# Kernel optimization log

Hardware: AMD Instinct MI355X
Metric: run time of the kernel (lower is better)

The kernel has to match this reference:

```python
import jax, jax.numpy as jnp
import numpy as np

GRID = 256

def _build_edges(g):
    ii, jj = np.meshgrid(np.arange(g), np.arange(g), indexing='ij')
    center = ii * g + jj
    srcs, tgts, attrs = [], [], []
    for di in (-1, 0, 1):
        for dj in (-1, 0, 1):
            if di == 0 and dj == 0:
                continue
            ni, nj = ii + di, jj + dj
            m = (ni >= 0) & (ni < g) & (nj >= 0) & (nj < g)
            srcs.append(center[m])
            tgts.append((ni * g + nj)[m])
            n = int(m.sum())
            a = np.empty((n, 3), np.float32)
            a[:, 0] = np.sqrt(di * di + dj * dj)
            a[:, 1] = di
            a[:, 2] = dj
            attrs.append(a)
    return (np.concatenate(srcs).astype(np.int32),
            np.concatenate(tgts).astype(np.int32),
            np.concatenate(attrs, axis=0))

def setup_inputs() -> dict:
    key = jax.random.key(0)
    ks = jax.random.split(key, 16)
    B, T, C, g = 2, 5, 10, GRID
    width, kw, out_c, Hh = 64, 32, 10, 32
    src, tgt, attr = _build_edges(g)
    nrm = lambda k, s: 0.1 * jax.random.normal(k, s, dtype=jnp.float32)
    return {
        'x': nrm(ks[0], (B, T, C, g, g)),
        'edge_src': jnp.asarray(src),
        'edge_tgt': jnp.asarray(tgt),
        'edge_attr': jnp.asarray(attr),
        'Wih0': nrm(ks[1], (4 * Hh, C)),
        'Whh0': nrm(ks[2], (4 * Hh, Hh)),
        'bih0': nrm(ks[3], (4 * Hh,)),
        'bhh0': nrm(ks[4], (4 * Hh,)),
        'Wih1': nrm(ks[5], (4 * Hh, Hh)),
        'Whh1': nrm(ks[6], (4 * Hh, Hh)),
        'bih1': nrm(ks[7], (4 * Hh,)),
        'bhh1': nrm(ks[8], (4 * Hh,)),
        'fc1_w': nrm(ks[9], (width, Hh)),
        'fc1_b': nrm(ks[10], (width,)),
        'conv_w': nrm(ks[11], (4, width, width)),
        'conv_b': nrm(ks[12], (4, width)),
        'gparam': jnp.ones((4,), jnp.float32),
        'fc2_w': nrm(ks[13], (kw, width)),
        'fc2_b': nrm(ks[14], (kw,)),
        'fc3_w': nrm(ks[15], (out_c, kw)),
        'fc3_b': jnp.zeros((out_c,), jnp.float32),
    }

def _lstm_cell(xt, h, c, Wih, Whh, bih, bhh):
    z = xt @ Wih.T + bih + h @ Whh.T + bhh
    i, f, g, o = jnp.split(z, 4, axis=-1)  # torch gate order i,f,g,o
    c = jax.nn.sigmoid(f) * c + jax.nn.sigmoid(i) * jnp.tanh(g)
    h = jax.nn.sigmoid(o) * jnp.tanh(c)
    return h, c

def _forward(x, edge_src, edge_tgt, edge_attr, Wih0, Whh0, bih0, bhh0,
             Wih1, Whh1, bih1, bhh1, fc1_w, fc1_b, conv_w, conv_b, gparam,
             fc2_w, fc2_b, fc3_w, fc3_b):
    B, T, C, H, W = x.shape
    N = H * W
    Hh = Whh0.shape[1]
    # (B,T,C,H,W) -> (T, B*N, C) sequence for the temporal LSTM over every node
    seq = x.transpose(0, 3, 4, 1, 2).reshape(B * N, T, C).transpose(1, 0, 2)

    def step(carry, xt):
        h0, c0, h1, c1 = carry
        h0, c0 = _lstm_cell(xt, h0, c0, Wih0, Whh0, bih0, bhh0)
        h1, c1 = _lstm_cell(h0, h1, c1, Wih1, Whh1, bih1, bhh1)
        return (h0, c0, h1, c1), None

    z = jnp.zeros((B * N, Hh), x.dtype)
    (h0, c0, h1, c1), _ = jax.lax.scan(step, (z, z, z, z), seq)
    feats = jax.nn.relu(h1 @ fc1_w.T + fc1_b).reshape(B, N, -1)  # (B,N,width)

    dist2 = edge_attr[:, 0:1] ** 2  # (E,1)
    depth = conv_w.shape[0]
    for k in range(depth):
        gw = jnp.exp(-dist2 / (gparam[k] ** 2 + 1e-8))       # (E,1) gaussian gate
        msg = (feats[:, edge_src] @ conv_w[k]) * gw          # (B,E,width)
        agg = jnp.zeros_like(feats).at[:, edge_tgt].add(msg) # scatter-add per batch
        feats = agg + feats @ conv_w[k] + conv_b[k]
        if k != depth - 1:
            feats = jax.nn.relu(feats)

    out = jax.nn.relu(feats @ fc2_w.T + fc2_b) @ fc3_w.T + fc3_b  # (B,N,out_c)
    out = out.reshape(B, H, W, -1).transpose(0, 3, 1, 2)[:, None]  # (B,1,out_c,H,W)
    return out

def reference(x, edge_src, edge_tgt, edge_attr, Wih0, Whh0, bih0, bhh0,
              Wih1, Whh1, bih1, bhh1, fc1_w, fc1_b, conv_w, conv_b, gparam,
              fc2_w, fc2_b, fc3_w, fc3_b):
    return _forward(x, edge_src, edge_tgt, edge_attr, Wih0, Whh0, bih0, bhh0,
                    Wih1, Whh1, bih1, bhh1, fc1_w, fc1_b, conv_w, conv_b, gparam,
                    fc2_w, fc2_b, fc3_w, fc3_b)
```

## Files before the change

### kernel.cpp

```cpp
#include <hip/hip_runtime.h>
#include <hip/hip_bf16.h>

#define NPIX   65536
#define TT     5
#define CC     10
#define HH     32
#define WIDTH  64
#define KW     32
#define OUTC   10

#define OFF_L0I    0
#define OFF_L0H    1280
#define OFF_L1I    5376
#define OFF_L1H    9472
#define OFF_B0     13568
#define OFF_B1     13696
#define OFF_FC1W   13824
#define OFF_FC1B   15872
#define OFF_CWT2   16384
#define OFF_CB     32768
#define OFF_FC2W2  33024
#define OFF_FC2B   35072
#define OFF_FC3W4  35104
#define OFF_FC3B   35424
#define OFF_GW     35440
#define OFF_FEATS_A 36864
#define OFF_FEATS_B (36864 + 8388608)

#define STRAIGHT_ATTR_IDX (65025 * 3)

__device__ __forceinline__ float sigf(float x)  { return 1.0f / (1.0f + __expf(-x)); }
__device__ __forceinline__ float tanhf_(float x){ return 1.0f - 2.0f / (__expf(2.0f * x) + 1.0f); }

__global__ __launch_bounds__(256, 1)
void prep_kernel(const float* Wih0, const float* Whh0,
                 const float* bih0, const float* bhh0,
                 const float* Wih1, const float* Whh1,
                 const float* bih1, const float* bhh1,
                 const float* fc1w, const float* fc1b,
                 const float* convw, const float* convb,
                 const float* fc2w, const float* fc2b,
                 const float* fc3w, const float* fc3b,
                 const float* gparam, const float* eattr,
                 float* P) {
    int tid = blockIdx.x * blockDim.x + threadIdx.x;
    int stride = gridDim.x * blockDim.x;
    for (int idx = tid; idx < 1280; idx += stride) {
        int g = idx & 3, j = (idx >> 2) & 31, c = idx >> 7;
        P[OFF_L0I + idx] = Wih0[(g * 32 + j) * 10 + c];
    }
    for (int idx = tid; idx < 4096; idx += stride) {
        int g = idx & 3, j = (idx >> 2) & 31, k = idx >> 7;
        P[OFF_L0H + idx] = Whh0[(g * 32 + j) * 32 + k];
        P[OFF_L1I + idx] = Wih1[(g * 32 + j) * 32 + k];
        P[OFF_L1H + idx] = Whh1[(g * 32 + j) * 32 + k];
    }
    for (int idx = tid; idx < 128; idx += stride) {
        int g = idx & 3, j = idx >> 2;
        P[OFF_B0 + idx] = bih0[g * 32 + j] + bhh0[g * 32 + j];
        P[OFF_B1 + idx] = bih1[g * 32 + j] + bhh1[g * 32 + j];
    }
    for (int idx = tid; idx < 2048; idx += stride) {
        int ch = idx & 63, k = idx >> 6;
        P[OFF_FC1W + idx] = fc1w[ch * 32 + k];
    }
    for (int i = tid; i < 64; i += stride) P[OFF_FC1B + i] = fc1b[i];
    for (int idx = tid; idx < 16384; idx += stride) {
        int k = idx >> 12, r = idx & 4095, e = r >> 1, h = r & 1;
        int co2 = e >> 6, ci = e & 63;
        P[OFF_CWT2 + idx] = convw[k * 4096 + ci * 64 + (2 * co2 + h)];
    }
    for (int i = tid; i < 256; i += stride) P[OFF_CB + i] = convb[i];
    for (int idx = tid; idx < 2048; idx += stride) {
        int e = idx >> 1, h = idx & 1, m2 = e >> 6, ch = e & 63;
        P[OFF_FC2W2 + idx] = fc2w[(2 * m2 + h) * 64 + ch];
    }
    for (int i = tid; i < 32;  i += stride) P[OFF_FC2B + i] = fc2b[i];
    for (int idx = tid; idx < 320; idx += stride) {
        int q = idx & 3, e = idx >> 2, oc2 = e >> 4, m2 = e & 15;
        int oc = 2 * oc2 + (q & 1), m = 2 * m2 + (q >> 1);
        P[OFF_FC3W4 + idx] = fc3w[oc * 32 + m];
    }
    for (int i = tid; i < 10; i += stride) P[OFF_FC3B + i] = fc3b[i];
    for (int idx = tid; idx < 8; idx += stride) {
        int k = idx >> 1;
        float g = gparam[k];
        float denom = g * g + 1e-8f;
        float a = (idx & 1) ? eattr[0] : eattr[STRAIGHT_ATTR_IDX];
        P[OFF_GW + idx] = __expf(-(a * a) / denom);
    }
}

#define ROW_ACC32(WBASE, SVAL) do {                                 \
    const float* wr_ = (WBASE); float sv_ = (SVAL);                 \
    _Pragma("unroll")                                               \
    for (int q_ = 0; q_ < 32; q_++)                                 \
        z[q_] = __builtin_fmaf(wr_[q_], sv_, z[q_]);                \
    } while (0)

__global__ __launch_bounds__(256, 1)
void lstm_fc1_kernel(const float* __restrict__ x,
                     const float* __restrict__ P,
                     float* __restrict__ feats) {
    __shared__ float H0[HH * 64];
    __shared__ float H1[HH * 64];

    int tid  = threadIdx.x;
    int w    = __builtin_amdgcn_readfirstlane(tid >> 6);
    int lane = tid & 63;
    int jw   = w << 3;
    int w32  = w << 5;

    int n = blockIdx.x * 64 + lane;
    int b = n >> 16;
    int pix = n & (NPIX - 1);
    const float* xb = x + (size_t)b * TT * CC * NPIX + pix;

    float c0[8], c1[8];
#pragma unroll
    for (int j = 0; j < 8; j++) {
        c0[j] = 0.f; c1[j] = 0.f;
        H0[(jw + j) * 64 + lane] = 0.f;
        H1[(jw + j) * 64 + lane] = 0.f;
    }
    __syncthreads();

#pragma unroll 1
    for (int t = 0; t < TT; t++) {
        float xcur[CC];
#pragma unroll
        for (int c = 0; c < CC; c++)
            xcur[c] = xb[(size_t)(t * CC + c) * NPIX];

        {
            float z[32];
            const float* bb = P + OFF_B0 + w32;
#pragma unroll
            for (int q = 0; q < 32; q++) z[q] = bb[q];
#pragma unroll 1
            for (int c = 0; c < CC; c++)
                ROW_ACC32(P + OFF_L0I + c * 128 + w32, xcur[c]);
#pragma unroll 1
            for (int k = 0; k < HH; k++) {
                float hv = H0[k * 64 + lane];
                ROW_ACC32(P + OFF_L0H + k * 128 + w32, hv);
            }
            __syncthreads();
#pragma unroll
            for (int j = 0; j < 8; j++) {
                float cn = sigf(z[4 * j + 1]) * c0[j]
                         + sigf(z[4 * j + 0]) * tanhf_(z[4 * j + 2]);
                c0[j] = cn;
                H0[(jw + j) * 64 + lane] = sigf(z[4 * j + 3]) * tanhf_(cn);
            }
            __syncthreads();
        }

        {
            float z[32];
            const float* bb = P + OFF_B1 + w32;
#pragma unroll
            for (int q = 0; q < 32; q++) z[q] = bb[q];
#pragma unroll 1
            for (int k = 0; k < HH; k++) {
                float hv = H0[k * 64 + lane];
                ROW_ACC32(P + OFF_L1I + k * 128 + w32, hv);
            }
#pragma unroll 1
            for (int k = 0; k < HH; k++) {
                float hv = H1[k * 64 + lane];
                ROW_ACC32(P + OFF_L1H + k * 128 + w32, hv);
            }
            __syncthreads();
#pragma unroll
            for (int j = 0; j < 8; j++) {
                float cn = sigf(z[4 * j + 1]) * c1[j]
                         + sigf(z[4 * j + 0]) * tanhf_(z[4 * j + 2]);
                c1[j] = cn;
                H1[(jw + j) * 64 + lane] = sigf(z[4 * j + 3]) * tanhf_(cn);
            }
            __syncthreads();
        }
    }

    float f[16];
    {
        const float* fb1 = P + OFF_FC1B + (w << 4);
#pragma unroll
        for (int m = 0; m < 16; m++) f[m] = fb1[m];
    }
#pragma unroll 1
    for (int k = 0; k < HH; k++) {
        float hv = H1[k * 64 + lane];
        const float* wr = P + OFF_FC1W + k * 64 + (w << 4);
#pragma unroll
        for (int m = 0; m < 16; m++)
            f[m] = __builtin_fmaf(wr[m], hv, f[m]);
    }
    float* fob = feats + (size_t)b * WIDTH * NPIX + (size_t)(w * 16) * NPIX + pix;
#pragma unroll
    for (int m = 0; m < 16; m++)
        fob[(size_t)m * NPIX] = fmaxf(f[m], 0.f);
}

__global__ __launch_bounds__(256, 1)
void conv_fused_kernel(const float* __restrict__ Fin, float* __restrict__ Fout,
                       const float* __restrict__ P, int k) {
    __shared__ float4 CW[1024];
    __shared__ float  CB[64];
    {
        const float4* src = (const float4*)(P + OFF_CWT2 + k * 4096);
        for (int i = threadIdx.x; i < 1024; i += 256) CW[i] = src[i];
        if (threadIdx.x < 64) CB[threadIdx.x] = P[OFF_CB + k * 64 + threadIdx.x];
    }
    __syncthreads();

    int n = blockIdx.x * 256 + threadIdx.x;
    int b = n >> 16;
    int pix = n & (NPIX - 1);
    int i = pix >> 8, j = pix & 255;
    float wstr = P[OFF_GW + 2 * k], wdiag = P[OFF_GW + 2 * k + 1];
    float fu = (i > 0) ? wstr : 0.f, fd = (i < 255) ? wstr : 0.f;
    float fl = (j > 0) ? wstr : 0.f, fr = (j < 255) ? wstr : 0.f;
    float ful = (i > 0 && j > 0) ? wdiag : 0.f, fur = (i > 0 && j < 255) ? wdiag : 0.f;
    float fdl = (i < 255 && j > 0) ? wdiag : 0.f, fdr = (i < 255 && j < 255) ? wdiag : 0.f;

    const float* fb = Fin + (size_t)b * WIDTH * NPIX + pix;
    float u[WIDTH];
#pragma unroll
    for (int ch = 0; ch < WIDTH; ch++) {
        const float* yc = fb + (size_t)ch * NPIX;
        float v = yc[0];
        v += fu * yc[-256] + fd * yc[256] + fl * yc[-1] + fr * yc[1];
        v += ful * yc[-257] + fur * yc[-255] + fdl * yc[255] + fdr * yc[257];
        u[ch] = v;
    }

    float* ob = Fout + (size_t)b * WIDTH * NPIX + pix;
#pragma unroll 1
    for (int co2 = 0; co2 < 32; co2++) {
        float ax = CB[2 * co2], ay = CB[2 * co2 + 1];
        const float4* wv = CW + co2 * 32;
#pragma unroll
        for (int ci2 = 0; ci2 < 32; ci2++) {
            float4 q = wv[ci2];
            float a0 = u[2 * ci2], a1 = u[2 * ci2 + 1];
            ax = __builtin_fmaf(q.x, a0, ax); ax = __builtin_fmaf(q.z, a1, ax);
            ay = __builtin_fmaf(q.y, a0, ay); ay = __builtin_fmaf(q.w, a1, ay);
        }
        ob[(size_t)(2 * co2) * NPIX]     = fmaxf(ax, 0.f);
        ob[(size_t)(2 * co2 + 1) * NPIX] = fmaxf(ay, 0.f);
    }
}

__global__ __launch_bounds__(256, 1)
void conv_head_kernel(const float* __restrict__ Fin, const float* __restrict__ P,
                      float* __restrict__ out) {
    const int k = 3;
    __shared__ float4 CW3[1024];
    __shared__ float  CB3[64];
    __shared__ float4 F2W[512];
    __shared__ float  F2B[32];
    __shared__ float4 F3W[80];
    __shared__ float  F3B[12];
    {
        const float4* s1 = (const float4*)(P + OFF_CWT2 + k * 4096);
        for (int i = threadIdx.x; i < 1024; i += 256) CW3[i] = s1[i];
        const float4* s2 = (const float4*)(P + OFF_FC2W2);
        for (int i = threadIdx.x; i < 512; i += 256) F2W[i] = s2[i];
        const float4* s3 = (const float4*)(P + OFF_FC3W4);
        if (threadIdx.x < 80) F3W[threadIdx.x] = s3[threadIdx.x];
        if (threadIdx.x < 64) CB3[threadIdx.x] = P[OFF_CB + k * 64 + threadIdx.x];
        if (threadIdx.x < 32) F2B[threadIdx.x] = P[OFF_FC2B + threadIdx.x];
        if (threadIdx.x < 10) F3B[threadIdx.x] = P[OFF_FC3B + threadIdx.x];
    }
    __syncthreads();

    int n = blockIdx.x * 256 + threadIdx.x;
    int b = n >> 16;
    int pix = n & (NPIX - 1);
    int i = pix >> 8, j = pix & 255;
    float wstr = P[OFF_GW + 2 * k], wdiag = P[OFF_GW + 2 * k + 1];
    float fu = (i > 0) ? wstr : 0.f, fd = (i < 255) ? wstr : 0.f;
    float fl = (j > 0) ? wstr : 0.f, fr = (j < 255) ? wstr : 0.f;
    float ful = (i > 0 && j > 0) ? wdiag : 0.f, fur = (i > 0 && j < 255) ? wdiag : 0.f;
    float fdl = (i < 255 && j > 0) ? wdiag : 0.f, fdr = (i < 255 && j < 255) ? wdiag : 0.f;

    const float* fb = Fin + (size_t)b * WIDTH * NPIX + pix;
    float u[WIDTH];
#pragma unroll
    for (int ch = 0; ch < WIDTH; ch++) {
        const float* yc = fb + (size_t)ch * NPIX;
        float v = yc[0];
        v += fu * yc[-256] + fd * yc[256] + fl * yc[-1] + fr * yc[1];
        v += ful * yc[-257] + fur * yc[-255] + fdl * yc[255] + fdr * yc[257];
        u[ch] = v;
    }

    float f[WIDTH];
#pragma unroll
    for (int co2 = 0; co2 < 32; co2++) {
        float ax = CB3[2 * co2], ay = CB3[2 * co2 + 1];
        const float4* wv = CW3 + co2 * 32;
#pragma unroll
        for (int ci2 = 0; ci2 < 32; ci2++) {
            float4 q = wv[ci2];
            float a0 = u[2 * ci2], a1 = u[2 * ci2 + 1];
            ax = __builtin_fmaf(q.x, a0, ax); ax = __builtin_fmaf(q.z, a1, ax);
            ay = __builtin_fmaf(q.y, a0, ay); ay = __builtin_fmaf(q.w, a1, ay);
        }
        f[2 * co2] = ax; f[2 * co2 + 1] = ay;
    }

    float2 oo[5];
#pragma unroll
    for (int oc2 = 0; oc2 < 5; oc2++) oo[oc2] = make_float2(F3B[2 * oc2], F3B[2 * oc2 + 1]);
#pragma unroll 1
    for (int m2 = 0; m2 < 16; m2++) {
        float ax = F2B[2 * m2], ay = F2B[2 * m2 + 1];
        const float4* wv = F2W + m2 * 32;
#pragma unroll
        for (int ch2 = 0; ch2 < 32; ch2++) {
            float4 q = wv[ch2];
            ax = __builtin_fmaf(q.x, f[2 * ch2], ax); ax = __builtin_fmaf(q.z, f[2 * ch2 + 1], ax);
            ay = __builtin_fmaf(q.y, f[2 * ch2], ay); ay = __builtin_fmaf(q.w, f[2 * ch2 + 1], ay);
        }
        ax = fmaxf(ax, 0.f); ay = fmaxf(ay, 0.f);
#pragma unroll
        for (int oc2 = 0; oc2 < 5; oc2++) {
            float4 q = F3W[oc2 * 16 + m2];
            oo[oc2].x += q.x * ax + q.z * ay;
            oo[oc2].y += q.y * ax + q.w * ay;
        }
    }
    float* ob = out + (size_t)b * OUTC * NPIX + pix;
#pragma unroll
    for (int oc2 = 0; oc2 < 5; oc2++) {
        ob[(size_t)(2 * oc2) * NPIX]     = oo[oc2].x;
        ob[(size_t)(2 * oc2 + 1) * NPIX] = oo[oc2].y;
    }
}

extern "C" void kernel_launch(void* const* d_in, const int* in_sizes, int n_in,
                              void* d_out, int out_size, void* d_ws, size_t ws_size,
                              hipStream_t stream) {
    const float* x     = (const float*)d_in[0];
    const float* eattr = (const float*)d_in[3];
    const float* Wih0  = (const float*)d_in[4];
    const float* Whh0  = (const float*)d_in[5];
    const float* bih0  = (const float*)d_in[6];
    const float* bhh0  = (const float*)d_in[7];
    const float* Wih1  = (const float*)d_in[8];
    const float* Whh1  = (const float*)d_in[9];
    const float* bih1  = (const float*)d_in[10];
    const float* bhh1  = (const float*)d_in[11];
    const float* fc1w  = (const float*)d_in[12];
    const float* fc1b  = (const float*)d_in[13];
    const float* convw = (const float*)d_in[14];
    const float* convb = (const float*)d_in[15];
    const float* gparam= (const float*)d_in[16];
    const float* fc2w  = (const float*)d_in[17];
    const float* fc2b  = (const float*)d_in[18];
    const float* fc3w  = (const float*)d_in[19];
    const float* fc3b  = (const float*)d_in[20];

    float* P  = (float*)d_ws;
    float* FA = P + OFF_FEATS_A;
    float* FB = P + OFF_FEATS_B;

    prep_kernel<<<64, 256, 0, stream>>>(Wih0, Whh0, bih0, bhh0, Wih1, Whh1, bih1, bhh1,
                                        fc1w, fc1b, convw, convb, fc2w, fc2b, fc3w, fc3b,
                                        gparam, eattr, P);
    lstm_fc1_kernel<<<2048, 256, 0, stream>>>(x, P, FA);
    conv_fused_kernel<<<512, 256, 0, stream>>>(FA, FB, P, 0);
    conv_fused_kernel<<<512, 256, 0, stream>>>(FB, FA, P, 1);
    conv_fused_kernel<<<512, 256, 0, stream>>>(FA, FB, P, 2);
    conv_head_kernel<<<512, 256, 0, stream>>>(FB, P, (float*)d_out);
}
```

Baseline: 593.3 us.

## Stage stencil outputs in LDS and register-tile the conv channel mix

The fused conv kernel now writes the 64-channel stencil result for its 256 pixels to shared memory, then each thread computes 16 output channels for 4 consecutive pixels, using float4 LDS reads and float4 global stores. Before, each thread held all 64 inputs in registers and read weights from LDS once per output pair. The new layout reuses each weight across 4 pixels and cuts register pressure, at the cost of 80KB of LDS per block, one extra barrier and a plain row-major weight layout. The head kernel now rebuilds its paired weight layout from the raw weights while loading them.

```diff
diff --git a/kernel.cpp b/kernel.cpp
--- a/kernel.cpp
+++ b/kernel.cpp
@@ -65,11 +65,8 @@
         P[OFF_FC1W + idx] = fc1w[ch * 32 + k];
     }
     for (int i = tid; i < 64; i += stride) P[OFF_FC1B + i] = fc1b[i];
-    for (int idx = tid; idx < 16384; idx += stride) {
-        int k = idx >> 12, r = idx & 4095, e = r >> 1, h = r & 1;
-        int co2 = e >> 6, ci = e & 63;
-        P[OFF_CWT2 + idx] = convw[k * 4096 + ci * 64 + (2 * co2 + h)];
-    }
+    for (int idx = tid; idx < 16384; idx += stride)
+        P[OFF_CWT2 + idx] = convw[idx];
     for (int i = tid; i < 256; i += stride) P[OFF_CB + i] = convb[i];
     for (int idx = tid; idx < 2048; idx += stride) {
         int e = idx >> 1, h = idx & 1, m2 = e >> 6, ch = e & 63;
@@ -206,16 +203,17 @@
 __global__ __launch_bounds__(256, 1)
 void conv_fused_kernel(const float* __restrict__ Fin, float* __restrict__ Fout,
                        const float* __restrict__ P, int k) {
-    __shared__ float4 CW[1024];
-    __shared__ float  CB[64];
+    __shared__ float US[64 * 256];
+    __shared__ float CW[64 * 64];
+
+    int tid = threadIdx.x;
     {
         const float4* src = (const float4*)(P + OFF_CWT2 + k * 4096);
-        for (int i = threadIdx.x; i < 1024; i += 256) CW[i] = src[i];
-        if (threadIdx.x < 64) CB[threadIdx.x] = P[OFF_CB + k * 64 + threadIdx.x];
-    }
-    __syncthreads();
-
-    int n = blockIdx.x * 256 + threadIdx.x;
+        float4* dst = (float4*)CW;
+        for (int idx = tid; idx < 1024; idx += 256) dst[idx] = src[idx];
+    }
+
+    int n = blockIdx.x * 256 + tid;
     int b = n >> 16;
     int pix = n & (NPIX - 1);
     int i = pix >> 8, j = pix & 255;
@@ -226,30 +224,61 @@
     float fdl = (i < 255 && j > 0) ? wdiag : 0.f, fdr = (i < 255 && j < 255) ? wdiag : 0.f;
 
     const float* fb = Fin + (size_t)b * WIDTH * NPIX + pix;
-    float u[WIDTH];
 #pragma unroll
     for (int ch = 0; ch < WIDTH; ch++) {
         const float* yc = fb + (size_t)ch * NPIX;
         float v = yc[0];
         v += fu * yc[-256] + fd * yc[256] + fl * yc[-1] + fr * yc[1];
         v += ful * yc[-257] + fur * yc[-255] + fdl * yc[255] + fdr * yc[257];
-        u[ch] = v;
-    }
-
-    float* ob = Fout + (size_t)b * WIDTH * NPIX + pix;
-#pragma unroll 1
-    for (int co2 = 0; co2 < 32; co2++) {
-        float ax = CB[2 * co2], ay = CB[2 * co2 + 1];
-        const float4* wv = CW + co2 * 32;
-#pragma unroll
-        for (int ci2 = 0; ci2 < 32; ci2++) {
-            float4 q = wv[ci2];
-            float a0 = u[2 * ci2], a1 = u[2 * ci2 + 1];
-            ax = __builtin_fmaf(q.x, a0, ax); ax = __builtin_fmaf(q.z, a1, ax);
-            ay = __builtin_fmaf(q.y, a0, ay); ay = __builtin_fmaf(q.w, a1, ay);
-        }
-        ob[(size_t)(2 * co2) * NPIX]     = fmaxf(ax, 0.f);
-        ob[(size_t)(2 * co2 + 1) * NPIX] = fmaxf(ay, 0.f);
+        US[ch * 256 + tid] = v;
+    }
+    __syncthreads();
+
+    int l = tid & 63;
+    int ob16 = (tid >> 6) << 4;
+    float4 acc[16];
+#pragma unroll
+    for (int o = 0; o < 16; o++) {
+        float bv = P[OFF_CB + k * 64 + ob16 + o];
+        acc[o] = make_float4(bv, bv, bv, bv);
+    }
+    const float4* US4 = (const float4*)US;
+#pragma unroll 1
+    for (int ci = 0; ci < 64; ci++) {
+        float4 u4 = US4[ci * 64 + l];
+        const float4* wr4 = (const float4*)(CW + ci * 64 + ob16);
+#pragma unroll
+        for (int q = 0; q < 4; q++) {
+            float4 wq = wr4[q];
+            acc[4 * q + 0].x = __builtin_fmaf(wq.x, u4.x, acc[4 * q + 0].x);
+            acc[4 * q + 0].y = __builtin_fmaf(wq.x, u4.y, acc[4 * q + 0].y);
+            acc[4 * q + 0].z = __builtin_fmaf(wq.x, u4.z, acc[4 * q + 0].z);
+            acc[4 * q + 0].w = __builtin_fmaf(wq.x, u4.w, acc[4 * q + 0].w);
+            acc[4 * q + 1].x = __builtin_fmaf(wq.y, u4.x, acc[4 * q + 1].x);
+            acc[4 * q + 1].y = __builtin_fmaf(wq.y, u4.y, acc[4 * q + 1].y);
+            acc[4 * q + 1].z = __builtin_fmaf(wq.y, u4.z, acc[4 * q + 1].z);
+            acc[4 * q + 1].w = __builtin_fmaf(wq.y, u4.w, acc[4 * q + 1].w);
+            acc[4 * q + 2].x = __builtin_fmaf(wq.z, u4.x, acc[4 * q + 2].x);
+            acc[4 * q + 2].y = __builtin_fmaf(wq.z, u4.y, acc[4 * q + 2].y);
+            acc[4 * q + 2].z = __builtin_fmaf(wq.z, u4.z, acc[4 * q + 2].z);
+            acc[4 * q + 2].w = __builtin_fmaf(wq.z, u4.w, acc[4 * q + 2].w);
+            acc[4 * q + 3].x = __builtin_fmaf(wq.w, u4.x, acc[4 * q + 3].x);
+            acc[4 * q + 3].y = __builtin_fmaf(wq.w, u4.y, acc[4 * q + 3].y);
+            acc[4 * q + 3].z = __builtin_fmaf(wq.w, u4.z, acc[4 * q + 3].z);
+            acc[4 * q + 3].w = __builtin_fmaf(wq.w, u4.w, acc[4 * q + 3].w);
+        }
+    }
+
+    int pn = blockIdx.x * 256 + 4 * l;
+    int pb = pn >> 16;
+    int ppix = pn & (NPIX - 1);
+    float* ob = Fout + (size_t)pb * WIDTH * NPIX + ppix;
+#pragma unroll
+    for (int o = 0; o < 16; o++) {
+        float4 r;
+        r.x = fmaxf(acc[o].x, 0.f); r.y = fmaxf(acc[o].y, 0.f);
+        r.z = fmaxf(acc[o].z, 0.f); r.w = fmaxf(acc[o].w, 0.f);
+        *(float4*)(ob + (size_t)(ob16 + o) * NPIX) = r;
     }
 }
 
@@ -264,8 +293,14 @@
     __shared__ float4 F3W[80];
     __shared__ float  F3B[12];
     {
-        const float4* s1 = (const float4*)(P + OFF_CWT2 + k * 4096);
-        for (int i = threadIdx.x; i < 1024; i += 256) CW3[i] = s1[i];
+        const float* wsrc = P + OFF_CWT2 + k * 4096;
+        for (int idx = threadIdx.x; idx < 1024; idx += 256) {
+            int co2 = idx >> 5, ci2 = idx & 31;
+            CW3[idx] = make_float4(wsrc[(2 * ci2) * 64 + 2 * co2],
+                                   wsrc[(2 * ci2) * 64 + 2 * co2 + 1],
+                                   wsrc[(2 * ci2 + 1) * 64 + 2 * co2],
+                                   wsrc[(2 * ci2 + 1) * 64 + 2 * co2 + 1]);
+        }
         const float4* s2 = (const float4*)(P + OFF_FC2W2);
         for (int i = threadIdx.x; i < 512; i += 256) F2W[i] = s2[i];
         const float4* s3 = (const float4*)(P + OFF_FC3W4);
```

New measurement: 566.0 us. -4.6%, faster.
